# Performance work log

Measured on AMD Instinct MI355X. Metric: run time of the kernel, lower is better.

Reference implementation:

```python
import jax, jax.numpy as jnp
import numpy as np

SCALE = 30.0
MARGIN = 0.4
H = 0.333
NUM_CLASSES = 100000
EMB = 512
BATCH = 512


def setup_inputs() -> dict:
    key = jax.random.key(0)
    k1, k2, k3 = jax.random.split(key, 3)
    embeddings = jax.random.normal(k1, (BATCH, EMB), dtype=jnp.float32)
    labels = jax.random.randint(k2, (BATCH,), 0, NUM_CLASSES, dtype=jnp.int64)
    # xavier_uniform: bound = sqrt(6 / (fan_in + fan_out)) with fan_in=EMB, fan_out=NUM_CLASSES
    bound = float(np.sqrt(6.0 / (EMB + NUM_CLASSES)))
    weight = jax.random.uniform(k3, (NUM_CLASSES, EMB), dtype=jnp.float32, minval=-bound, maxval=bound)
    return {"embeddings": embeddings, "labels": labels, "weight": weight}


def reference(embeddings, labels, weight):
    n = embeddings.shape[0]
    rows = jnp.arange(n)

    emb_norm = jnp.linalg.norm(embeddings, axis=1, keepdims=True)      # [N,1]
    w_unit = weight / jnp.linalg.norm(weight, axis=1, keepdims=True)   # [C,D]
    emb_unit = embeddings / emb_norm                                   # [N,D]
    cosine = emb_unit @ w_unit.T                                       # [N,C]

    batch_mean = jnp.mean(emb_norm)
    batch_std = jnp.std(emb_norm, ddof=1)  # torch.std is unbiased
    margin_scaler = jnp.clip((emb_norm - batch_mean) / (batch_std + H), -1.0, 1.0)  # [N,1]
    adaptive_margin = MARGIN * (1.0 + margin_scaler[:, 0])             # [N]

    # Apply angular margin only at the label position (equivalent to the
    # one_hot scatter + where in the original, without a second N x C pass).
    cos_t = cosine[rows, labels]                                       # [N]
    cos_t_m = jnp.cos(jnp.arccos(cos_t) + adaptive_margin)             # [N]
    logits = SCALE * cosine.at[rows, labels].set(cos_t_m)              # [N,C]

    # cross-entropy with mean reduction
    lse = jax.nn.logsumexp(logits, axis=1)                             # [N]
    loss = jnp.mean(lse - logits[rows, labels])
    return loss
```

## Files before the change

kernel.cpp:

```cpp
#include <hip/hip_runtime.h>
#include <hip/hip_bf16.h>

#define C_NUM 100000
#define D_EMB 512
#define N_BATCH 512
#define SCALE_F 30.0f
#define MARGIN_F 0.4f
#define H_F 0.333f
#define NT2 782
#define NCH 16

typedef __attribute__((ext_vector_type(8))) short bf16x8;
typedef __attribute__((ext_vector_type(4))) short bf16x4;
typedef __attribute__((ext_vector_type(4))) float f32x4;
typedef __attribute__((ext_vector_type(16))) float f32x16;

static __device__ __forceinline__ short f2bf(float f) {
  __hip_bfloat16 h = __float2bfloat16(f);
  union { __hip_bfloat16 b; short s; } u;
  u.b = h;
  return u.s;
}

static __device__ __forceinline__ float sq4(f32x4 v) {
  return v[0]*v[0] + v[1]*v[1] + v[2]*v[2] + v[3]*v[3];
}

static __device__ __forceinline__ void gload16(const void* g, void* l) {
  __builtin_amdgcn_global_load_lds(
      (const __attribute__((address_space(1))) void*)g,
      (__attribute__((address_space(3))) void*)l, 16, 0, 0);
}

__global__ __launch_bounds__(64) void k_rownorm(const float* __restrict__ emb,
                                                short* __restrict__ Aunit,
                                                float* __restrict__ norms) {
  const int i = blockIdx.x;
  const int l = threadIdx.x;
  const f32x4* row = reinterpret_cast<const f32x4*>(emb + (size_t)i * D_EMB);
  f32x4 v0 = row[l];
  f32x4 v1 = row[l + 64];
  float ss = sq4(v0) + sq4(v1);
#pragma unroll
  for (int m = 1; m < 64; m <<= 1) ss += __shfl_xor(ss, m);
  float nrm = sqrtf(ss);
  float inv = 1.0f / nrm;
  bf16x4 o0, o1;
#pragma unroll
  for (int q = 0; q < 4; ++q) { o0[q] = f2bf(v0[q] * inv); o1[q] = f2bf(v1[q] * inv); }
  bf16x4* dst = reinterpret_cast<bf16x4*>(Aunit + (size_t)i * D_EMB);
  dst[l] = o0;
  dst[l + 64] = o1;
  if (l == 0) norms[i] = nrm;
}

__global__ __launch_bounds__(512) void k_stats(const float* __restrict__ norms,
                                               float* __restrict__ marg) {
  __shared__ float red[8];
  const int t = threadIdx.x;
  const int lane = t & 63, wid = t >> 6;
  float x = norms[t];
  float s = x;
#pragma unroll
  for (int m = 1; m < 64; m <<= 1) s += __shfl_xor(s, m);
  if (lane == 0) red[wid] = s;
  __syncthreads();
  float tot = 0.f;
#pragma unroll
  for (int q = 0; q < 8; ++q) tot += red[q];
  const float mean = tot / 512.f;
  __syncthreads();
  float d = x - mean;
  float s2 = d * d;
#pragma unroll
  for (int m = 1; m < 64; m <<= 1) s2 += __shfl_xor(s2, m);
  if (lane == 0) red[wid] = s2;
  __syncthreads();
  float tot2 = 0.f;
#pragma unroll
  for (int q = 0; q < 8; ++q) tot2 += red[q];
  const float stdv = sqrtf(tot2 / 511.f);
  float msc = (x - mean) / (stdv + H_F);
  msc = fminf(1.f, fmaxf(-1.f, msc));
  marg[t] = MARGIN_F * (1.f + msc);
}

__global__ __launch_bounds__(256, 3) void k_main(const short* __restrict__ Aunit,
                                                 const float* __restrict__ weight,
                                                 const int* __restrict__ labels,
                                                 const float* __restrict__ marg,
                                                 float* __restrict__ partial,
                                                 float* __restrict__ tlogit) {
  __shared__ alignas(16) char As[2][8192];
  __shared__ alignas(16) char Ws[2][10240];
  __shared__ float winv[128];

  const int bid = blockIdx.x;
  const int grp = bid >> 5, within = bid & 31;
  const int rt = (within >> 3) & 3;
  const int ct = grp * 8 + (within & 7);
  if (ct >= NT2) return;

  const int tid = threadIdx.x;
  const int w = tid >> 6, lane = tid & 63;
  const int l31 = lane & 31, lhi = lane >> 5;

  const int ar0 = w * 32 + (lane >> 2);
  const int ak0 = ((lane & 3) * 16) ^ (((ar0 >> 1) & 3) << 4);
  const char* gAb0 = (const char*)Aunit + (size_t)(rt * 128 + ar0) * 1024 + ak0;
  const char* gAb1 = gAb0 + (size_t)16 * 1024;

  const int sc8 = tid >> 3;
  const int su  = tid & 7;
  const float* wbase0; const float* wbase1; const float* wbase2; const float* wbase3;
  int wdst0, wdst1, wdst2, wdst3;
  {
    int c0 = 0 * 32 + sc8, c1 = 1 * 32 + sc8, c2 = 2 * 32 + sc8, c3 = 3 * 32 + sc8;
    int g0 = ct * 128 + c0; if (g0 > C_NUM - 1) g0 = C_NUM - 1;
    int g1 = ct * 128 + c1; if (g1 > C_NUM - 1) g1 = C_NUM - 1;
    int g2 = ct * 128 + c2; if (g2 > C_NUM - 1) g2 = C_NUM - 1;
    int g3 = ct * 128 + c3; if (g3 > C_NUM - 1) g3 = C_NUM - 1;
    wbase0 = weight + (size_t)g0 * D_EMB + su * 4;
    wbase1 = weight + (size_t)g1 * D_EMB + su * 4;
    wbase2 = weight + (size_t)g2 * D_EMB + su * 4;
    wbase3 = weight + (size_t)g3 * D_EMB + su * 4;
    wdst0 = c0 * 80 + su * 8; wdst1 = c1 * 80 + su * 8;
    wdst2 = c2 * 80 + su * 8; wdst3 = c3 * 80 + su * 8;
  }

  const int xa = ((l31 >> 1) & 3) << 4;
  const int abase = (w * 32 + l31) * 64;

  f32x16 acc0, acc1, acc2, acc3;
#pragma unroll
  for (int q = 0; q < 16; ++q) { acc0[q] = 0.f; acc1[q] = 0.f; acc2[q] = 0.f; acc3[q] = 0.f; }
  float ssq0 = 0.f, ssq1 = 0.f, ssq2 = 0.f, ssq3 = 0.f;

  f32x4 pa0, pa1, pa2, pa3;
  f32x4 pb0, pb1, pb2, pb3;

#define WLOAD(R0,R1,R2,R3,OFF) { \
    R0 = *(const f32x4*)(wbase0 + (OFF)); R1 = *(const f32x4*)(wbase1 + (OFF)); \
    R2 = *(const f32x4*)(wbase2 + (OFF)); R3 = *(const f32x4*)(wbase3 + (OFF)); }

#define WWRITE(BUF,R0,R1,R2,R3) { \
    bf16x4 t0, t1, t2, t3; \
    _Pragma("unroll") \
    for (int e = 0; e < 4; ++e) { t0[e] = f2bf(R0[e]); t1[e] = f2bf(R1[e]); \
                                  t2[e] = f2bf(R2[e]); t3[e] = f2bf(R3[e]); } \
    *(bf16x4*)(&Ws[BUF][wdst0]) = t0; *(bf16x4*)(&Ws[BUF][wdst1]) = t1; \
    *(bf16x4*)(&Ws[BUF][wdst2]) = t2; *(bf16x4*)(&Ws[BUF][wdst3]) = t3; }

#define SSQADD(R0,R1,R2,R3) { ssq0 += sq4(R0); ssq1 += sq4(R1); \
                              ssq2 += sq4(R2); ssq3 += sq4(R3); }

#define COMPUTE(BUF) { \
    const char* Ab = As[BUF]; const char* Wb = Ws[BUF]; \
    __builtin_amdgcn_s_setprio(1); \
    _Pragma("unroll") \
    for (int kk = 0; kk < 2; ++kk) { \
      const int kb = kk * 32 + lhi * 16; \
      bf16x8 a  = *(const bf16x8*)(Ab + abase + (kb ^ xa)); \
      bf16x8 b0 = *(const bf16x8*)(Wb + (l31)      * 80 + kb); \
      bf16x8 b1 = *(const bf16x8*)(Wb + (32 + l31) * 80 + kb); \
      bf16x8 b2 = *(const bf16x8*)(Wb + (64 + l31) * 80 + kb); \
      bf16x8 b3 = *(const bf16x8*)(Wb + (96 + l31) * 80 + kb); \
      acc0 = __builtin_amdgcn_mfma_f32_32x32x16_bf16(a, b0, acc0, 0, 0, 0); \
      acc1 = __builtin_amdgcn_mfma_f32_32x32x16_bf16(a, b1, acc1, 0, 0, 0); \
      acc2 = __builtin_amdgcn_mfma_f32_32x32x16_bf16(a, b2, acc2, 0, 0, 0); \
      acc3 = __builtin_amdgcn_mfma_f32_32x32x16_bf16(a, b3, acc3, 0, 0, 0); \
    } \
    __builtin_amdgcn_s_setprio(0); }

  WLOAD(pa0, pa1, pa2, pa3, 0);
  __builtin_amdgcn_sched_barrier(0);
  gload16(gAb0, &As[0][w * 2048]);
  gload16(gAb1, &As[0][w * 2048 + 1024]);
  __builtin_amdgcn_sched_barrier(0);
  WLOAD(pb0, pb1, pb2, pb3, 32);
  __builtin_amdgcn_sched_barrier(0);
  asm volatile("s_waitcnt vmcnt(4)" ::: "memory");
  SSQADD(pa0, pa1, pa2, pa3);
  WWRITE(0, pa0, pa1, pa2, pa3);
  asm volatile("s_waitcnt lgkmcnt(0)" ::: "memory");
  __builtin_amdgcn_s_barrier();
  __builtin_amdgcn_sched_barrier(0);

  for (int i = 0; i < 8; ++i) {
    {
      const int ao = (2 * i + 1) * 64;
      gload16(gAb0 + ao, &As[1][w * 2048]);
      gload16(gAb1 + ao, &As[1][w * 2048 + 1024]);
      __builtin_amdgcn_sched_barrier(0);
      int cw = 2 * i + 2; if (cw > 15) cw = 15;
      WLOAD(pa0, pa1, pa2, pa3, cw * 32);
      __builtin_amdgcn_sched_barrier(0);
      COMPUTE(0);
      asm volatile("s_waitcnt vmcnt(4)" ::: "memory");
      SSQADD(pb0, pb1, pb2, pb3);
      WWRITE(1, pb0, pb1, pb2, pb3);
      asm volatile("s_waitcnt lgkmcnt(0)" ::: "memory");
      __builtin_amdgcn_s_barrier();
      __builtin_amdgcn_sched_barrier(0);
    }
    {
      int ca = 2 * i + 2; if (ca > 15) ca = 15;
      const int ao = ca * 64;
      gload16(gAb0 + ao, &As[0][w * 2048]);
      gload16(gAb1 + ao, &As[0][w * 2048 + 1024]);
      __builtin_amdgcn_sched_barrier(0);
      int cw = 2 * i + 3; if (cw > 15) cw = 15;
      WLOAD(pb0, pb1, pb2, pb3, cw * 32);
      __builtin_amdgcn_sched_barrier(0);
      COMPUTE(1);
      asm volatile("s_waitcnt vmcnt(4)" ::: "memory");
      if (2 * i + 2 <= 15) SSQADD(pa0, pa1, pa2, pa3);
      WWRITE(0, pa0, pa1, pa2, pa3);
      asm volatile("s_waitcnt lgkmcnt(0)" ::: "memory");
      __builtin_amdgcn_s_barrier();
      __builtin_amdgcn_sched_barrier(0);
    }
  }

  {
    float s0 = ssq0, s1 = ssq1, s2 = ssq2, s3 = ssq3;
#pragma unroll
    for (int m = 1; m < 8; m <<= 1) {
      s0 += __shfl_xor(s0, m); s1 += __shfl_xor(s1, m);
      s2 += __shfl_xor(s2, m); s3 += __shfl_xor(s3, m);
    }
    if (su == 0) {
      winv[sc8]      = (s0 > 0.f) ? rsqrtf(s0) : 0.f;
      winv[32 + sc8] = (s1 > 0.f) ? rsqrtf(s1) : 0.f;
      winv[64 + sc8] = (s2 > 0.f) ? rsqrtf(s2) : 0.f;
      winv[96 + sc8] = (s3 > 0.f) ? rsqrtf(s3) : 0.f;
    }
  }
  __syncthreads();

  const float wv0 = winv[l31];
  const float wv1 = winv[32 + l31];
  const float wv2 = winv[64 + l31];
  const float wv3 = winv[96 + l31];
  const int cb = ct * 128;
#pragma unroll
  for (int r = 0; r < 16; ++r) {
    const int rowf = (r & 3) + 8 * (r >> 2) + 4 * lhi;
    const int R = rt * 128 + w * 32 + rowf;
    const int lab = labels[R];
    float v = 0.f;
#pragma unroll
    for (int ni = 0; ni < 4; ++ni) {
      const int gcc = cb + ni * 32 + l31;
      const float wv = (ni == 0) ? wv0 : (ni == 1) ? wv1 : (ni == 2) ? wv2 : wv3;
      const float av = (ni == 0) ? acc0[r] : (ni == 1) ? acc1[r] : (ni == 2) ? acc2[r] : acc3[r];
      const float cosv = av * wv;
      float lg = SCALE_F * cosv;
      if (lab == gcc) {
        float ctv = fminf(1.f, fmaxf(-1.f, cosv));
        float lt = SCALE_F * cosf(acosf(ctv) + marg[R]);
        lg = lt;
        tlogit[R] = lt;
      }
      v += (gcc < C_NUM) ? __expf(lg) : 0.f;
    }
    v += __shfl_xor(v, 1);
    v += __shfl_xor(v, 2);
    v += __shfl_xor(v, 4);
    v += __shfl_xor(v, 8);
    v += __shfl_xor(v, 16);
    if (l31 == 0) partial[(size_t)ct * N_BATCH + R] = v;
  }
#undef WLOAD
#undef WWRITE
#undef SSQADD
#undef COMPUTE
}

__global__ __launch_bounds__(64) void k_reduce(const float* __restrict__ partial,
                                               const float* __restrict__ tlogit,
                                               float* __restrict__ term) {
  const int r = blockIdx.x;
  const int l = threadIdx.x;
  float s = 0.f;
  for (int b = l; b < NT2; b += 64)
    s += partial[(size_t)b * N_BATCH + r];
#pragma unroll
  for (int m = 1; m < 64; m <<= 1) s += __shfl_xor(s, m);
  if (l == 0) term[r] = logf(s) - tlogit[r];
}

__global__ __launch_bounds__(512) void k_final(const float* __restrict__ term,
                                               float* __restrict__ out) {
  __shared__ float red[8];
  const int t = threadIdx.x;
  const int lane = t & 63, wid = t >> 6;
  float v = term[t];
#pragma unroll
  for (int m = 1; m < 64; m <<= 1) v += __shfl_xor(v, m);
  if (lane == 0) red[wid] = v;
  __syncthreads();
  if (t == 0) {
    float tot = 0.f;
#pragma unroll
    for (int q = 0; q < 8; ++q) tot += red[q];
    out[0] = tot / 512.f;
  }
}

extern "C" void kernel_launch(void* const* d_in, const int* in_sizes, int n_in,
                              void* d_out, int out_size, void* d_ws, size_t ws_size,
                              hipStream_t stream) {
  const float* emb    = (const float*)d_in[0];
  const int*   labels = (const int*)d_in[1];
  const float* weight = (const float*)d_in[2];
  float* out = (float*)d_out;

  char* ws = (char*)d_ws;
  short* Aunit   = (short*)ws;
  float* norms   = (float*)(ws + 524288);
  float* marg    = (float*)(ws + 524288 + 2048);
  float* tlog    = (float*)(ws + 524288 + 4096);
  float* term    = (float*)(ws + 524288 + 6144);
  float* partial = (float*)(ws + 524288 + 8192);

  k_rownorm<<<N_BATCH, 64, 0, stream>>>(emb, Aunit, norms);
  k_stats<<<1, 512, 0, stream>>>(norms, marg);
  k_main<<<98 * 32, 256, 0, stream>>>(Aunit, weight, labels, marg, partial, tlog);
  k_reduce<<<N_BATCH, 64, 0, stream>>>(partial, tlog, term);
  k_final<<<1, 512, 0, stream>>>(term, out);
}
```

Measured before the change: 134.6 us.

## Load embedding tiles directly into registers instead of staging through LDS

```diff
diff --git a/kernel.cpp b/kernel.cpp
--- a/kernel.cpp
+++ b/kernel.cpp
@@ -24,12 +24,6 @@
 
 static __device__ __forceinline__ float sq4(f32x4 v) {
   return v[0]*v[0] + v[1]*v[1] + v[2]*v[2] + v[3]*v[3];
-}
-
-static __device__ __forceinline__ void gload16(const void* g, void* l) {
-  __builtin_amdgcn_global_load_lds(
-      (const __attribute__((address_space(1))) void*)g,
-      (__attribute__((address_space(3))) void*)l, 16, 0, 0);
 }
 
 __global__ __launch_bounds__(64) void k_rownorm(const float* __restrict__ emb,
@@ -85,13 +79,12 @@
   marg[t] = MARGIN_F * (1.f + msc);
 }
 
-__global__ __launch_bounds__(256, 3) void k_main(const short* __restrict__ Aunit,
+__global__ __launch_bounds__(256, 4) void k_main(const short* __restrict__ Aunit,
                                                  const float* __restrict__ weight,
                                                  const int* __restrict__ labels,
                                                  const float* __restrict__ marg,
                                                  float* __restrict__ partial,
                                                  float* __restrict__ tlogit) {
-  __shared__ alignas(16) char As[2][8192];
   __shared__ alignas(16) char Ws[2][10240];
   __shared__ float winv[128];
 
@@ -105,10 +98,7 @@
   const int w = tid >> 6, lane = tid & 63;
   const int l31 = lane & 31, lhi = lane >> 5;
 
-  const int ar0 = w * 32 + (lane >> 2);
-  const int ak0 = ((lane & 3) * 16) ^ (((ar0 >> 1) & 3) << 4);
-  const char* gAb0 = (const char*)Aunit + (size_t)(rt * 128 + ar0) * 1024 + ak0;
-  const char* gAb1 = gAb0 + (size_t)16 * 1024;
+  const char* arow = (const char*)Aunit + (size_t)(rt * 128 + w * 32 + l31) * 1024 + lhi * 16;
 
   const int sc8 = tid >> 3;
   const int su  = tid & 7;
@@ -128,9 +118,6 @@
     wdst2 = c2 * 80 + su * 8; wdst3 = c3 * 80 + su * 8;
   }
 
-  const int xa = ((l31 >> 1) & 3) << 4;
-  const int abase = (w * 32 + l31) * 64;
-
   f32x16 acc0, acc1, acc2, acc3;
 #pragma unroll
   for (int q = 0; q < 16; ++q) { acc0[q] = 0.f; acc1[q] = 0.f; acc2[q] = 0.f; acc3[q] = 0.f; }
@@ -154,28 +141,36 @@
 #define SSQADD(R0,R1,R2,R3) { ssq0 += sq4(R0); ssq1 += sq4(R1); \
                               ssq2 += sq4(R2); ssq3 += sq4(R3); }
 
-#define COMPUTE(BUF) { \
-    const char* Ab = As[BUF]; const char* Wb = Ws[BUF]; \
+#define COMPUTE(BUF,CHUNK) { \
+    const char* Wb = Ws[BUF]; \
+    bf16x8 a0 = *(const bf16x8*)(arow + (CHUNK) * 64); \
+    bf16x8 a1 = *(const bf16x8*)(arow + (CHUNK) * 64 + 32); \
     __builtin_amdgcn_s_setprio(1); \
-    _Pragma("unroll") \
-    for (int kk = 0; kk < 2; ++kk) { \
-      const int kb = kk * 32 + lhi * 16; \
-      bf16x8 a  = *(const bf16x8*)(Ab + abase + (kb ^ xa)); \
+    { \
+      const int kb = lhi * 16; \
       bf16x8 b0 = *(const bf16x8*)(Wb + (l31)      * 80 + kb); \
       bf16x8 b1 = *(const bf16x8*)(Wb + (32 + l31) * 80 + kb); \
       bf16x8 b2 = *(const bf16x8*)(Wb + (64 + l31) * 80 + kb); \
       bf16x8 b3 = *(const bf16x8*)(Wb + (96 + l31) * 80 + kb); \
-      acc0 = __builtin_amdgcn_mfma_f32_32x32x16_bf16(a, b0, acc0, 0, 0, 0); \
-      acc1 = __builtin_amdgcn_mfma_f32_32x32x16_bf16(a, b1, acc1, 0, 0, 0); \
-      acc2 = __builtin_amdgcn_mfma_f32_32x32x16_bf16(a, b2, acc2, 0, 0, 0); \
-      acc3 = __builtin_amdgcn_mfma_f32_32x32x16_bf16(a, b3, acc3, 0, 0, 0); \
+      acc0 = __builtin_amdgcn_mfma_f32_32x32x16_bf16(a0, b0, acc0, 0, 0, 0); \
+      acc1 = __builtin_amdgcn_mfma_f32_32x32x16_bf16(a0, b1, acc1, 0, 0, 0); \
+      acc2 = __builtin_amdgcn_mfma_f32_32x32x16_bf16(a0, b2, acc2, 0, 0, 0); \
+      acc3 = __builtin_amdgcn_mfma_f32_32x32x16_bf16(a0, b3, acc3, 0, 0, 0); \
+    } \
+    { \
+      const int kb = 32 + lhi * 16; \
+      bf16x8 b0 = *(const bf16x8*)(Wb + (l31)      * 80 + kb); \
+      bf16x8 b1 = *(const bf16x8*)(Wb + (32 + l31) * 80 + kb); \
+      bf16x8 b2 = *(const bf16x8*)(Wb + (64 + l31) * 80 + kb); \
+      bf16x8 b3 = *(const bf16x8*)(Wb + (96 + l31) * 80 + kb); \
+      acc0 = __builtin_amdgcn_mfma_f32_32x32x16_bf16(a1, b0, acc0, 0, 0, 0); \
+      acc1 = __builtin_amdgcn_mfma_f32_32x32x16_bf16(a1, b1, acc1, 0, 0, 0); \
+      acc2 = __builtin_amdgcn_mfma_f32_32x32x16_bf16(a1, b2, acc2, 0, 0, 0); \
+      acc3 = __builtin_amdgcn_mfma_f32_32x32x16_bf16(a1, b3, acc3, 0, 0, 0); \
     } \
     __builtin_amdgcn_s_setprio(0); }
 
   WLOAD(pa0, pa1, pa2, pa3, 0);
-  __builtin_amdgcn_sched_barrier(0);
-  gload16(gAb0, &As[0][w * 2048]);
-  gload16(gAb1, &As[0][w * 2048 + 1024]);
   __builtin_amdgcn_sched_barrier(0);
   WLOAD(pb0, pb1, pb2, pb3, 32);
   __builtin_amdgcn_sched_barrier(0);
@@ -188,14 +183,10 @@
 
   for (int i = 0; i < 8; ++i) {
     {
-      const int ao = (2 * i + 1) * 64;
-      gload16(gAb0 + ao, &As[1][w * 2048]);
-      gload16(gAb1 + ao, &As[1][w * 2048 + 1024]);
-      __builtin_amdgcn_sched_barrier(0);
       int cw = 2 * i + 2; if (cw > 15) cw = 15;
       WLOAD(pa0, pa1, pa2, pa3, cw * 32);
       __builtin_amdgcn_sched_barrier(0);
-      COMPUTE(0);
+      COMPUTE(0, 2 * i);
       asm volatile("s_waitcnt vmcnt(4)" ::: "memory");
       SSQADD(pb0, pb1, pb2, pb3);
       WWRITE(1, pb0, pb1, pb2, pb3);
@@ -204,15 +195,10 @@
       __builtin_amdgcn_sched_barrier(0);
     }
     {
-      int ca = 2 * i + 2; if (ca > 15) ca = 15;
-      const int ao = ca * 64;
-      gload16(gAb0 + ao, &As[0][w * 2048]);
-      gload16(gAb1 + ao, &As[0][w * 2048 + 1024]);
-      __builtin_amdgcn_sched_barrier(0);
       int cw = 2 * i + 3; if (cw > 15) cw = 15;
       WLOAD(pb0, pb1, pb2, pb3, cw * 32);
       __builtin_amdgcn_sched_barrier(0);
-      COMPUTE(1);
+      COMPUTE(1, 2 * i + 1);
       asm volatile("s_waitcnt vmcnt(4)" ::: "memory");
       if (2 * i + 2 <= 15) SSQADD(pa0, pa1, pa2, pa3);
       WWRITE(0, pa0, pa1, pa2, pa3);
```

After: 421.0 us. 3.13x slower.

## Halve class tile width to 64 and transpose partial-sum layout

Applied to the files above, without the earlier changes.

```diff
diff --git a/kernel.cpp b/kernel.cpp
--- a/kernel.cpp
+++ b/kernel.cpp
@@ -7,7 +7,8 @@
 #define SCALE_F 30.0f
 #define MARGIN_F 0.4f
 #define H_F 0.333f
-#define NT2 782
+#define NT64 1563
+#define PST 1568
 #define NCH 16
 
 typedef __attribute__((ext_vector_type(8))) short bf16x8;
@@ -85,21 +86,21 @@
   marg[t] = MARGIN_F * (1.f + msc);
 }
 
-__global__ __launch_bounds__(256, 3) void k_main(const short* __restrict__ Aunit,
+__global__ __launch_bounds__(256, 5) void k_main(const short* __restrict__ Aunit,
                                                  const float* __restrict__ weight,
                                                  const int* __restrict__ labels,
                                                  const float* __restrict__ marg,
                                                  float* __restrict__ partial,
                                                  float* __restrict__ tlogit) {
   __shared__ alignas(16) char As[2][8192];
-  __shared__ alignas(16) char Ws[2][10240];
-  __shared__ float winv[128];
+  __shared__ alignas(16) char Ws[2][5120];
+  __shared__ float winv[64];
 
   const int bid = blockIdx.x;
   const int grp = bid >> 5, within = bid & 31;
   const int rt = (within >> 3) & 3;
   const int ct = grp * 8 + (within & 7);
-  if (ct >= NT2) return;
+  if (ct >= NT64) return;
 
   const int tid = threadIdx.x;
   const int w = tid >> 6, lane = tid & 63;
@@ -110,51 +111,39 @@
   const char* gAb0 = (const char*)Aunit + (size_t)(rt * 128 + ar0) * 1024 + ak0;
   const char* gAb1 = gAb0 + (size_t)16 * 1024;
 
-  const int sc8 = tid >> 3;
-  const int su  = tid & 7;
-  const float* wbase0; const float* wbase1; const float* wbase2; const float* wbase3;
-  int wdst0, wdst1, wdst2, wdst3;
+  const int sc4 = tid >> 2;
+  const int su  = tid & 3;
+  const float* wbase;
+  int wdst;
   {
-    int c0 = 0 * 32 + sc8, c1 = 1 * 32 + sc8, c2 = 2 * 32 + sc8, c3 = 3 * 32 + sc8;
-    int g0 = ct * 128 + c0; if (g0 > C_NUM - 1) g0 = C_NUM - 1;
-    int g1 = ct * 128 + c1; if (g1 > C_NUM - 1) g1 = C_NUM - 1;
-    int g2 = ct * 128 + c2; if (g2 > C_NUM - 1) g2 = C_NUM - 1;
-    int g3 = ct * 128 + c3; if (g3 > C_NUM - 1) g3 = C_NUM - 1;
-    wbase0 = weight + (size_t)g0 * D_EMB + su * 4;
-    wbase1 = weight + (size_t)g1 * D_EMB + su * 4;
-    wbase2 = weight + (size_t)g2 * D_EMB + su * 4;
-    wbase3 = weight + (size_t)g3 * D_EMB + su * 4;
-    wdst0 = c0 * 80 + su * 8; wdst1 = c1 * 80 + su * 8;
-    wdst2 = c2 * 80 + su * 8; wdst3 = c3 * 80 + su * 8;
+    int gcl = ct * 64 + sc4; if (gcl > C_NUM - 1) gcl = C_NUM - 1;
+    wbase = weight + (size_t)gcl * D_EMB + su * 8;
+    wdst  = sc4 * 80 + su * 16;
   }
 
   const int xa = ((l31 >> 1) & 3) << 4;
   const int abase = (w * 32 + l31) * 64;
 
-  f32x16 acc0, acc1, acc2, acc3;
-#pragma unroll
-  for (int q = 0; q < 16; ++q) { acc0[q] = 0.f; acc1[q] = 0.f; acc2[q] = 0.f; acc3[q] = 0.f; }
-  float ssq0 = 0.f, ssq1 = 0.f, ssq2 = 0.f, ssq3 = 0.f;
-
-  f32x4 pa0, pa1, pa2, pa3;
-  f32x4 pb0, pb1, pb2, pb3;
-
-#define WLOAD(R0,R1,R2,R3,OFF) { \
-    R0 = *(const f32x4*)(wbase0 + (OFF)); R1 = *(const f32x4*)(wbase1 + (OFF)); \
-    R2 = *(const f32x4*)(wbase2 + (OFF)); R3 = *(const f32x4*)(wbase3 + (OFF)); }
-
-#define WWRITE(BUF,R0,R1,R2,R3) { \
-    bf16x4 t0, t1, t2, t3; \
+  f32x16 acc0, acc1;
+#pragma unroll
+  for (int q = 0; q < 16; ++q) { acc0[q] = 0.f; acc1[q] = 0.f; }
+  float ssq = 0.f;
+
+  f32x4 pa0, pa1;
+  f32x4 pb0, pb1;
+
+#define WLOAD(R0,R1,OFF) { \
+    R0 = *(const f32x4*)(wbase + (OFF)); R1 = *(const f32x4*)(wbase + (OFF) + 4); }
+
+#define WWRITE(BUF,R0,R1) { \
+    bf16x8 t0; \
     _Pragma("unroll") \
-    for (int e = 0; e < 4; ++e) { t0[e] = f2bf(R0[e]); t1[e] = f2bf(R1[e]); \
-                                  t2[e] = f2bf(R2[e]); t3[e] = f2bf(R3[e]); } \
-    *(bf16x4*)(&Ws[BUF][wdst0]) = t0; *(bf16x4*)(&Ws[BUF][wdst1]) = t1; \
-    *(bf16x4*)(&Ws[BUF][wdst2]) = t2; *(bf16x4*)(&Ws[BUF][wdst3]) = t3; }
-
-#define SSQADD(R0,R1,R2,R3) { ssq0 += sq4(R0); ssq1 += sq4(R1); \
-                              ssq2 += sq4(R2); ssq3 += sq4(R3); }
-
-#define COMPUTE(BUF) { \
+    for (int e = 0; e < 4; ++e) { t0[e] = f2bf(R0[e]); t0[e + 4] = f2bf(R1[e]); } \
+    *(bf16x8*)(&Ws[BUF][wdst]) = t0; }
+
+#define SSQADD(R0,R1) { ssq += sq4(R0) + sq4(R1); }
+
+#define COMPUTE(BUF,CHUNK) { \
     const char* Ab = As[BUF]; const char* Wb = Ws[BUF]; \
     __builtin_amdgcn_s_setprio(1); \
     _Pragma("unroll") \
@@ -163,25 +152,21 @@
       bf16x8 a  = *(const bf16x8*)(Ab + abase + (kb ^ xa)); \
       bf16x8 b0 = *(const bf16x8*)(Wb + (l31)      * 80 + kb); \
       bf16x8 b1 = *(const bf16x8*)(Wb + (32 + l31) * 80 + kb); \
-      bf16x8 b2 = *(const bf16x8*)(Wb + (64 + l31) * 80 + kb); \
-      bf16x8 b3 = *(const bf16x8*)(Wb + (96 + l31) * 80 + kb); \
       acc0 = __builtin_amdgcn_mfma_f32_32x32x16_bf16(a, b0, acc0, 0, 0, 0); \
       acc1 = __builtin_amdgcn_mfma_f32_32x32x16_bf16(a, b1, acc1, 0, 0, 0); \
-      acc2 = __builtin_amdgcn_mfma_f32_32x32x16_bf16(a, b2, acc2, 0, 0, 0); \
-      acc3 = __builtin_amdgcn_mfma_f32_32x32x16_bf16(a, b3, acc3, 0, 0, 0); \
     } \
     __builtin_amdgcn_s_setprio(0); }
 
-  WLOAD(pa0, pa1, pa2, pa3, 0);
+  WLOAD(pa0, pa1, 0);
   __builtin_amdgcn_sched_barrier(0);
   gload16(gAb0, &As[0][w * 2048]);
   gload16(gAb1, &As[0][w * 2048 + 1024]);
   __builtin_amdgcn_sched_barrier(0);
-  WLOAD(pb0, pb1, pb2, pb3, 32);
+  WLOAD(pb0, pb1, 32);
   __builtin_amdgcn_sched_barrier(0);
-  asm volatile("s_waitcnt vmcnt(4)" ::: "memory");
-  SSQADD(pa0, pa1, pa2, pa3);
-  WWRITE(0, pa0, pa1, pa2, pa3);
+  asm volatile("s_waitcnt vmcnt(2)" ::: "memory");
+  SSQADD(pa0, pa1);
+  WWRITE(0, pa0, pa1);
   asm volatile("s_waitcnt lgkmcnt(0)" ::: "memory");
   __builtin_amdgcn_s_barrier();
   __builtin_amdgcn_sched_barrier(0);
@@ -193,12 +178,12 @@
       gload16(gAb1 + ao, &As[1][w * 2048 + 1024]);
       __builtin_amdgcn_sched_barrier(0);
       int cw = 2 * i + 2; if (cw > 15) cw = 15;
-      WLOAD(pa0, pa1, pa2, pa3, cw * 32);
-      __builtin_amdgcn_sched_barrier(0);
-      COMPUTE(0);
-      asm volatile("s_waitcnt vmcnt(4)" ::: "memory");
-      SSQADD(pb0, pb1, pb2, pb3);
-      WWRITE(1, pb0, pb1, pb2, pb3);
+      WLOAD(pa0, pa1, cw * 32);
+      __builtin_amdgcn_sched_barrier(0);
+      COMPUTE(0, 2 * i);
+      asm volatile("s_waitcnt vmcnt(2)" ::: "memory");
+      SSQADD(pb0, pb1);
+      WWRITE(1, pb0, pb1);
       asm volatile("s_waitcnt lgkmcnt(0)" ::: "memory");
       __builtin_amdgcn_s_barrier();
       __builtin_amdgcn_sched_barrier(0);
@@ -210,12 +195,12 @@
       gload16(gAb1 + ao, &As[0][w * 2048 + 1024]);
       __builtin_amdgcn_sched_barrier(0);
       int cw = 2 * i + 3; if (cw > 15) cw = 15;
-      WLOAD(pb0, pb1, pb2, pb3, cw * 32);
-      __builtin_amdgcn_sched_barrier(0);
-      COMPUTE(1);
-      asm volatile("s_waitcnt vmcnt(4)" ::: "memory");
-      if (2 * i + 2 <= 15) SSQADD(pa0, pa1, pa2, pa3);
-      WWRITE(0, pa0, pa1, pa2, pa3);
+      WLOAD(pb0, pb1, cw * 32);
+      __builtin_amdgcn_sched_barrier(0);
+      COMPUTE(1, 2 * i + 1);
+      asm volatile("s_waitcnt vmcnt(2)" ::: "memory");
+      if (2 * i + 2 <= 15) SSQADD(pa0, pa1);
+      WWRITE(0, pa0, pa1);
       asm volatile("s_waitcnt lgkmcnt(0)" ::: "memory");
       __builtin_amdgcn_s_barrier();
       __builtin_amdgcn_sched_barrier(0);
@@ -223,53 +208,46 @@
   }
 
   {
-    float s0 = ssq0, s1 = ssq1, s2 = ssq2, s3 = ssq3;
-#pragma unroll
-    for (int m = 1; m < 8; m <<= 1) {
-      s0 += __shfl_xor(s0, m); s1 += __shfl_xor(s1, m);
-      s2 += __shfl_xor(s2, m); s3 += __shfl_xor(s3, m);
-    }
-    if (su == 0) {
-      winv[sc8]      = (s0 > 0.f) ? rsqrtf(s0) : 0.f;
-      winv[32 + sc8] = (s1 > 0.f) ? rsqrtf(s1) : 0.f;
-      winv[64 + sc8] = (s2 > 0.f) ? rsqrtf(s2) : 0.f;
-      winv[96 + sc8] = (s3 > 0.f) ? rsqrtf(s3) : 0.f;
-    }
+    float s = ssq;
+    s += __shfl_xor(s, 1);
+    s += __shfl_xor(s, 2);
+    if (su == 0) winv[sc4] = (s > 0.f) ? rsqrtf(s) : 0.f;
   }
   __syncthreads();
 
   const float wv0 = winv[l31];
   const float wv1 = winv[32 + l31];
-  const float wv2 = winv[64 + l31];
-  const float wv3 = winv[96 + l31];
-  const int cb = ct * 128;
+  const int cb = ct * 64;
+  const int gcc0 = cb + l31;
+  const int gcc1 = cb + 32 + l31;
+  const bool ok0 = gcc0 < C_NUM;
+  const bool ok1 = gcc1 < C_NUM;
 #pragma unroll
   for (int r = 0; r < 16; ++r) {
     const int rowf = (r & 3) + 8 * (r >> 2) + 4 * lhi;
     const int R = rt * 128 + w * 32 + rowf;
     const int lab = labels[R];
-    float v = 0.f;
-#pragma unroll
-    for (int ni = 0; ni < 4; ++ni) {
-      const int gcc = cb + ni * 32 + l31;
-      const float wv = (ni == 0) ? wv0 : (ni == 1) ? wv1 : (ni == 2) ? wv2 : wv3;
-      const float av = (ni == 0) ? acc0[r] : (ni == 1) ? acc1[r] : (ni == 2) ? acc2[r] : acc3[r];
-      const float cosv = av * wv;
-      float lg = SCALE_F * cosv;
-      if (lab == gcc) {
-        float ctv = fminf(1.f, fmaxf(-1.f, cosv));
-        float lt = SCALE_F * cosf(acosf(ctv) + marg[R]);
-        lg = lt;
-        tlogit[R] = lt;
-      }
-      v += (gcc < C_NUM) ? __expf(lg) : 0.f;
+    const float c0v = acc0[r] * wv0;
+    const float c1v = acc1[r] * wv1;
+    float lg0 = SCALE_F * c0v;
+    float lg1 = SCALE_F * c1v;
+    if (lab == gcc0) {
+      float ctv = fminf(1.f, fmaxf(-1.f, c0v));
+      float lt = SCALE_F * cosf(acosf(ctv) + marg[R]);
+      lg0 = lt; tlogit[R] = lt;
     }
+    if (lab == gcc1) {
+      float ctv = fminf(1.f, fmaxf(-1.f, c1v));
+      float lt = SCALE_F * cosf(acosf(ctv) + marg[R]);
+      lg1 = lt; tlogit[R] = lt;
+    }
+    float v = (ok0 ? __expf(lg0) : 0.f) + (ok1 ? __expf(lg1) : 0.f);
     v += __shfl_xor(v, 1);
     v += __shfl_xor(v, 2);
     v += __shfl_xor(v, 4);
     v += __shfl_xor(v, 8);
     v += __shfl_xor(v, 16);
-    if (l31 == 0) partial[(size_t)ct * N_BATCH + R] = v;
+    if (l31 == 0) partial[(size_t)R * PST + ct] = v;
   }
 #undef WLOAD
 #undef WWRITE
@@ -282,9 +260,10 @@
                                                float* __restrict__ term) {
   const int r = blockIdx.x;
   const int l = threadIdx.x;
+  const float* row = partial + (size_t)r * PST;
   float s = 0.f;
-  for (int b = l; b < NT2; b += 64)
-    s += partial[(size_t)b * N_BATCH + r];
+  for (int b = l; b < NT64; b += 64)
+    s += row[b];
 #pragma unroll
   for (int m = 1; m < 64; m <<= 1) s += __shfl_xor(s, m);
   if (l == 0) term[r] = logf(s) - tlogit[r];
@@ -326,7 +305,8 @@
 
   k_rownorm<<<N_BATCH, 64, 0, stream>>>(emb, Aunit, norms);
   k_stats<<<1, 512, 0, stream>>>(norms, marg);
-  k_main<<<98 * 32, 256, 0, stream>>>(Aunit, weight, labels, marg, partial, tlog);
+  const int ngrp = (NT64 + 7) / 8;
+  k_main<<<ngrp * 32, 256, 0, stream>>>(Aunit, weight, labels, marg, partial, tlog);
   k_reduce<<<N_BATCH, 64, 0, stream>>>(partial, tlog, term);
   k_final<<<1, 512, 0, stream>>>(term, out);
 }
```

New measurement: 432.8 us. +221.4%, slower.
